# Kernel optimization log

Measured on AMD Instinct MI355X. Metric: run time of the kernel, lower is better.

The kernel has to match this reference:

```python
import jax, jax.numpy as jnp
import numpy as np

WINDOW_SIZE = 64
SHIFT_SIZE = WINDOW_SIZE // 2  # shift_windows=True
HEAD_DIM = 64
SCALE = HEAD_DIM ** (-0.5)


def _shift_mask(W):
    # static shift-window mask, computed with numpy (all shapes static)
    img_mask = np.zeros((W,), dtype=np.float32)
    cnt = 0
    for s in (slice(0, -WINDOW_SIZE), slice(-WINDOW_SIZE, -SHIFT_SIZE), slice(-SHIFT_SIZE, None)):
        img_mask[s] = cnt
        cnt += 1
    mw = img_mask.reshape(W // WINDOW_SIZE, WINDOW_SIZE)  # (num_win, ws)
    mask = mw[:, None, :] - mw[:, :, None]                # (num_win, ws, ws)
    mask = np.where(mask != 0.0, -100.0, 0.0).astype(np.float32)
    return jnp.asarray(mask)


def setup_inputs() -> dict:
    key = jax.random.key(0)
    k1, k2, k3, k4 = jax.random.split(key, 4)
    B, W, C = 32, 8192, HEAD_DIM
    return {
        "q": jax.random.normal(k1, (B, W, C), dtype=jnp.float32),
        "k": jax.random.normal(k2, (B, W, C), dtype=jnp.float32),
        "v": jax.random.normal(k3, (B, W, C), dtype=jnp.float32),
        "rel_pos_table": jax.random.normal(k4, (2 * WINDOW_SIZE - 1, 1), dtype=jnp.float32) * 0.02,
    }


def reference(q, k, v, rel_pos_table):
    B, W, C = q.shape
    ws = WINDOW_SIZE
    # relative position bias gather: (1, ws, ws)
    coords = jnp.arange(ws)
    rel_idx = coords[None, :] * 0 + (coords[:, None] - coords[None, :]) + (ws - 1)  # (ws, ws)
    bias = rel_pos_table[rel_idx.reshape(-1)].reshape(ws, ws, -1)
    bias = jnp.transpose(bias, (2, 0, 1))  # (1, ws, ws)

    mask = _shift_mask(W)  # (num_win, ws, ws)

    # cyclic shift
    q = jnp.roll(q, shift=-SHIFT_SIZE, axis=1)
    k = jnp.roll(k, shift=-SHIFT_SIZE, axis=1)
    v = jnp.roll(v, shift=-SHIFT_SIZE, axis=1)

    # window partition -> (B * num_win, ws, C)
    num_win = W // ws
    qw = q.reshape(B * num_win, ws, C)
    kw = k.reshape(B * num_win, ws, C)
    vw = v.reshape(B * num_win, ws, C)

    attn = jnp.einsum('bnc,bmc->bnm', qw, kw) * SCALE + bias  # (B*nw, ws, ws)
    attn = attn.reshape(B, num_win, ws, ws) + mask[None]
    attn = attn.reshape(-1, ws, ws)
    attn = jax.nn.softmax(attn, axis=-1)

    xw = jnp.einsum('bnm,bmc->bnc', attn, vw)  # (B*nw, ws, C)
    x = xw.reshape(B, W, C)
    x = jnp.roll(x, shift=SHIFT_SIZE, axis=1)
    return (x, attn)
```

## Files before the change

kernel.cpp:

```cpp
#include <hip/hip_runtime.h>
#include <cstdint>
#include <cstddef>

#define WS 64
#define SHIFT 32
#define WTOT 8192
#define NWIN 128
#define SCALE_F 0.125f

typedef __bf16 bf16x8 __attribute__((ext_vector_type(8)));
typedef float f32x4 __attribute__((ext_vector_type(4)));

__device__ __forceinline__ unsigned short f2bf(float f) {
  unsigned int u = __builtin_bit_cast(unsigned int, f);
  u += 0x7FFFu + ((u >> 16) & 1u);
  return (unsigned short)(u >> 16);
}
__device__ __forceinline__ float bf2f(unsigned short h) {
  unsigned int u = ((unsigned int)h) << 16;
  return __builtin_bit_cast(float, u);
}

__global__ __launch_bounds__(256, 3) void win_attn(
    const float* __restrict__ q, const float* __restrict__ k,
    const float* __restrict__ v, const float* __restrict__ table,
    float* __restrict__ xout, float* __restrict__ attn_out) {
  __shared__ __align__(16) unsigned short s_qhi[WS * WS];
  __shared__ __align__(16) unsigned short s_qlo[WS * WS];
  __shared__ __align__(16) unsigned short s_khi[WS * WS];
  __shared__ __align__(16) unsigned short s_klo[WS * WS];
  __shared__ __align__(16) unsigned short s_vthi[WS * WS];
  __shared__ __align__(16) unsigned short s_vtlo[WS * WS];
  __shared__ float s_bias[2 * WS - 1];

  const int t = threadIdx.x;
  const int b = blockIdx.x;
  const int batch = b >> 7;
  const int win = b & (NWIN - 1);

  if (t < 2 * WS - 1) s_bias[t] = table[t];

  {
    const int lr = t >> 2;
    const int lc = (t & 3) << 4;
    const int grow = (win * WS + lr + SHIFT) & (WTOT - 1);
    const size_t gbase = ((size_t)batch * WTOT + grow) * WS + lc;
#pragma unroll
    for (int i = 0; i < 16; i += 4) {
      const float4 qv = *(const float4*)(q + gbase + i);
      const float4 kv = *(const float4*)(k + gbase + i);
      const float4 vv = *(const float4*)(v + gbase + i);
      const float qa[4] = {qv.x, qv.y, qv.z, qv.w};
      const float ka[4] = {kv.x, kv.y, kv.z, kv.w};
      const float va[4] = {vv.x, vv.y, vv.z, vv.w};
#pragma unroll
      for (int e = 0; e < 4; ++e) {
        const int cc = lc + i + e;
        unsigned short h;
        h = f2bf(qa[e]);
        s_qhi[lr * WS + cc] = h;
        s_qlo[lr * WS + cc] = f2bf(qa[e] - bf2f(h));
        h = f2bf(ka[e]);
        s_khi[lr * WS + cc] = h;
        s_klo[lr * WS + cc] = f2bf(ka[e] - bf2f(h));
        h = f2bf(va[e]);
        s_vthi[cc * WS + lr] = h;
        s_vtlo[cc * WS + lr] = f2bf(va[e] - bf2f(h));
      }
    }
  }
  __syncthreads();

  const int lane = t & 63;
  const int wave = t >> 6;
  const int lrow = lane & 15;
  const int quad = lane >> 4;

  const f32x4 z4 = {0.f, 0.f, 0.f, 0.f};
  f32x4 acc[4] = {z4, z4, z4, z4};
#pragma unroll
  for (int kh = 0; kh < 2; ++kh) {
    const int k0 = kh * 32 + quad * 8;
    const bf16x8 ahi = *(const bf16x8*)(s_qhi + (wave * 16 + lrow) * WS + k0);
    const bf16x8 alo = *(const bf16x8*)(s_qlo + (wave * 16 + lrow) * WS + k0);
#pragma unroll
    for (int j = 0; j < 4; ++j) {
      const bf16x8 bhi = *(const bf16x8*)(s_khi + (j * 16 + lrow) * WS + k0);
      const bf16x8 blo = *(const bf16x8*)(s_klo + (j * 16 + lrow) * WS + k0);
      acc[j] = __builtin_amdgcn_mfma_f32_16x16x32_bf16(ahi, bhi, acc[j], 0, 0, 0);
      acc[j] = __builtin_amdgcn_mfma_f32_16x16x32_bf16(alo, bhi, acc[j], 0, 0, 0);
      acc[j] = __builtin_amdgcn_mfma_f32_16x16x32_bf16(ahi, blo, acc[j], 0, 0, 0);
    }
  }

  const bool masked = (win == NWIN - 1);
  float p[4][4];
#pragma unroll
  for (int reg = 0; reg < 4; ++reg) {
    const int r = wave * 16 + quad * 4 + reg;
    float val[4];
    float vmax = -1e30f;
#pragma unroll
    for (int j = 0; j < 4; ++j) {
      const int m = j * 16 + lrow;
      float s = acc[j][reg] * SCALE_F + s_bias[r - m + (WS - 1)];
      if (masked && (((r ^ m) & 32) != 0)) s -= 100.0f;
      val[j] = s;
      vmax = fmaxf(vmax, s);
    }
#pragma unroll
    for (int off = 1; off < 16; off <<= 1)
      vmax = fmaxf(vmax, __shfl_xor(vmax, off, 64));
    float sum = 0.f;
#pragma unroll
    for (int j = 0; j < 4; ++j) {
      val[j] = __expf(val[j] - vmax);
      sum += val[j];
    }
#pragma unroll
    for (int off = 1; off < 16; off <<= 1)
      sum += __shfl_xor(sum, off, 64);
    const float inv = 1.0f / sum;
#pragma unroll
    for (int j = 0; j < 4; ++j) p[reg][j] = val[j] * inv;
  }

  {
    float* arow = attn_out + (size_t)b * (WS * WS);
#pragma unroll
    for (int reg = 0; reg < 4; ++reg) {
      const int r = wave * 16 + quad * 4 + reg;
#pragma unroll
      for (int j = 0; j < 4; ++j) {
        const int m = j * 16 + lrow;
        const float pv = p[reg][j];
        arow[r * WS + m] = pv;
        const unsigned short h = f2bf(pv);
        s_qhi[r * WS + m] = h;
        s_qlo[r * WS + m] = f2bf(pv - bf2f(h));
      }
    }
  }
  __syncthreads();

  f32x4 xacc[4] = {z4, z4, z4, z4};
#pragma unroll
  for (int kh = 0; kh < 2; ++kh) {
    const int k0 = kh * 32 + quad * 8;
    const bf16x8 phi = *(const bf16x8*)(s_qhi + (wave * 16 + lrow) * WS + k0);
    const bf16x8 plo = *(const bf16x8*)(s_qlo + (wave * 16 + lrow) * WS + k0);
#pragma unroll
    for (int j = 0; j < 4; ++j) {
      const bf16x8 vhi = *(const bf16x8*)(s_vthi + (j * 16 + lrow) * WS + k0);
      const bf16x8 vlo = *(const bf16x8*)(s_vtlo + (j * 16 + lrow) * WS + k0);
      xacc[j] = __builtin_amdgcn_mfma_f32_16x16x32_bf16(phi, vhi, xacc[j], 0, 0, 0);
      xacc[j] = __builtin_amdgcn_mfma_f32_16x16x32_bf16(plo, vhi, xacc[j], 0, 0, 0);
      xacc[j] = __builtin_amdgcn_mfma_f32_16x16x32_bf16(phi, vlo, xacc[j], 0, 0, 0);
    }
  }

#pragma unroll
  for (int reg = 0; reg < 4; ++reg) {
    const int r = wave * 16 + quad * 4 + reg;
    const int gr = (win * WS + r + SHIFT) & (WTOT - 1);
    float* xrow = xout + ((size_t)batch * WTOT + gr) * WS;
#pragma unroll
    for (int j = 0; j < 4; ++j) {
      xrow[j * 16 + lrow] = xacc[j][reg];
    }
  }
}

extern "C" void kernel_launch(void* const* d_in, const int* in_sizes, int n_in,
                              void* d_out, int out_size, void* d_ws, size_t ws_size,
                              hipStream_t stream) {
  (void)in_sizes; (void)n_in; (void)out_size; (void)d_ws; (void)ws_size;
  const float* q = (const float*)d_in[0];
  const float* k = (const float*)d_in[1];
  const float* v = (const float*)d_in[2];
  const float* table = (const float*)d_in[3];
  float* xout = (float*)d_out;
  float* attn = (float*)d_out + (size_t)32 * WTOT * WS;
  win_attn<<<dim3(4096), dim3(256), 0, stream>>>(q, k, v, table, xout, attn);
}
```

Baseline: 284.0 us.

## Load Q directly into registers, pad LDS rows, truncate bf16 split, nontemporal stores

Q fragments are loaded from global memory straight into MFMA operand registers, so Q no longer goes through shared memory and the LDS footprint shrinks. K and V^T hi/lo tiles use a padded row stride to reduce bank conflicts, and K is written with vectorized 16-byte stores. The bf16 hi/lo split now truncates instead of rounding, which cuts conversion ALU work. The P matrix reuses the K buffer after a barrier, the target occupancy is raised to 4 blocks per CU, and output and attention stores are nontemporal. Truncation slightly changes the split-precision error, and global Q loads become per-lane 32-byte strided reads.

```diff
diff --git a/kernel.cpp b/kernel.cpp
--- a/kernel.cpp
+++ b/kernel.cpp
@@ -7,30 +7,38 @@
 #define WTOT 8192
 #define NWIN 128
 #define SCALE_F 0.125f
+#define LDS_STRIDE 72
 
 typedef __bf16 bf16x8 __attribute__((ext_vector_type(8)));
+typedef unsigned short u16x8 __attribute__((ext_vector_type(8)));
 typedef float f32x4 __attribute__((ext_vector_type(4)));
 
-__device__ __forceinline__ unsigned short f2bf(float f) {
-  unsigned int u = __builtin_bit_cast(unsigned int, f);
-  u += 0x7FFFu + ((u >> 16) & 1u);
-  return (unsigned short)(u >> 16);
-}
-__device__ __forceinline__ float bf2f(unsigned short h) {
-  unsigned int u = ((unsigned int)h) << 16;
-  return __builtin_bit_cast(float, u);
-}
-
-__global__ __launch_bounds__(256, 3) void win_attn(
+__device__ __forceinline__ void split1(float f, unsigned short& h, unsigned short& l) {
+  const unsigned u = __builtin_bit_cast(unsigned, f);
+  h = (unsigned short)(u >> 16);
+  const float hf = __builtin_bit_cast(float, u & 0xFFFF0000u);
+  const float r = f - hf;
+  l = (unsigned short)(__builtin_bit_cast(unsigned, r) >> 16);
+}
+
+__device__ __forceinline__ void split8(const float* f, bf16x8& hi, bf16x8& lo) {
+  u16x8 hv, lv;
+#pragma unroll
+  for (int e = 0; e < 8; ++e) {
+    unsigned short hh, ll;
+    split1(f[e], hh, ll);
+    hv[e] = hh; lv[e] = ll;
+  }
+  hi = __builtin_bit_cast(bf16x8, hv);
+  lo = __builtin_bit_cast(bf16x8, lv);
+}
+
+__global__ __launch_bounds__(256, 4) void win_attn(
     const float* __restrict__ q, const float* __restrict__ k,
     const float* __restrict__ v, const float* __restrict__ table,
     float* __restrict__ xout, float* __restrict__ attn_out) {
-  __shared__ __align__(16) unsigned short s_qhi[WS * WS];
-  __shared__ __align__(16) unsigned short s_qlo[WS * WS];
-  __shared__ __align__(16) unsigned short s_khi[WS * WS];
-  __shared__ __align__(16) unsigned short s_klo[WS * WS];
-  __shared__ __align__(16) unsigned short s_vthi[WS * WS];
-  __shared__ __align__(16) unsigned short s_vtlo[WS * WS];
+  __shared__ __align__(16) unsigned short s_k[2][WS * LDS_STRIDE];
+  __shared__ __align__(16) unsigned short s_vt[2][WS * LDS_STRIDE];
   __shared__ float s_bias[2 * WS - 1];
 
   const int t = threadIdx.x;
@@ -38,55 +46,73 @@
   const int batch = b >> 7;
   const int win = b & (NWIN - 1);
 
-  if (t < 2 * WS - 1) s_bias[t] = table[t];
-
-  {
-    const int lr = t >> 2;
-    const int lc = (t & 3) << 4;
-    const int grow = (win * WS + lr + SHIFT) & (WTOT - 1);
-    const size_t gbase = ((size_t)batch * WTOT + grow) * WS + lc;
-#pragma unroll
-    for (int i = 0; i < 16; i += 4) {
-      const float4 qv = *(const float4*)(q + gbase + i);
-      const float4 kv = *(const float4*)(k + gbase + i);
-      const float4 vv = *(const float4*)(v + gbase + i);
-      const float qa[4] = {qv.x, qv.y, qv.z, qv.w};
-      const float ka[4] = {kv.x, kv.y, kv.z, kv.w};
-      const float va[4] = {vv.x, vv.y, vv.z, vv.w};
-#pragma unroll
-      for (int e = 0; e < 4; ++e) {
-        const int cc = lc + i + e;
-        unsigned short h;
-        h = f2bf(qa[e]);
-        s_qhi[lr * WS + cc] = h;
-        s_qlo[lr * WS + cc] = f2bf(qa[e] - bf2f(h));
-        h = f2bf(ka[e]);
-        s_khi[lr * WS + cc] = h;
-        s_klo[lr * WS + cc] = f2bf(ka[e] - bf2f(h));
-        h = f2bf(va[e]);
-        s_vthi[cc * WS + lr] = h;
-        s_vtlo[cc * WS + lr] = f2bf(va[e] - bf2f(h));
-      }
-    }
-  }
-  __syncthreads();
-
   const int lane = t & 63;
   const int wave = t >> 6;
   const int lrow = lane & 15;
   const int quad = lane >> 4;
 
+  if (t < 2 * WS - 1) s_bias[t] = table[t];
+
+  bf16x8 aq_hi[2], aq_lo[2];
+  {
+    const int qrow = wave * 16 + lrow;
+    const int gq = (win * WS + qrow + SHIFT) & (WTOT - 1);
+    const float* qp = q + ((size_t)batch * WTOT + gq) * WS;
+#pragma unroll
+    for (int kh = 0; kh < 2; ++kh) {
+      const float4 f0 = *(const float4*)(qp + kh * 32 + quad * 8);
+      const float4 f1 = *(const float4*)(qp + kh * 32 + quad * 8 + 4);
+      const float fa[8] = {f0.x, f0.y, f0.z, f0.w, f1.x, f1.y, f1.z, f1.w};
+      split8(fa, aq_hi[kh], aq_lo[kh]);
+    }
+  }
+
+  {
+    const int lr = t >> 2;
+    const int gk = (win * WS + lr + SHIFT) & (WTOT - 1);
+    const size_t gbase = ((size_t)batch * WTOT + gk) * WS;
+
+    const int lck = (t & 3) << 4;
+    const float* kp = k + gbase + lck;
+#pragma unroll
+    for (int g = 0; g < 2; ++g) {
+      const float4 f0 = *(const float4*)(kp + g * 8);
+      const float4 f1 = *(const float4*)(kp + g * 8 + 4);
+      const float fa[8] = {f0.x, f0.y, f0.z, f0.w, f1.x, f1.y, f1.z, f1.w};
+      bf16x8 hi, lo;
+      split8(fa, hi, lo);
+      *(bf16x8*)(&s_k[0][lr * LDS_STRIDE + lck + g * 8]) = hi;
+      *(bf16x8*)(&s_k[1][lr * LDS_STRIDE + lck + g * 8]) = lo;
+    }
+
+    const int cv = (t & 3) << 2;
+#pragma unroll
+    for (int blk = 0; blk < 4; ++blk) {
+      const float4 vv = *(const float4*)(v + gbase + cv + blk * 16);
+      const float va[4] = {vv.x, vv.y, vv.z, vv.w};
+#pragma unroll
+      for (int e = 0; e < 4; ++e) {
+        const int cc = cv + blk * 16 + e;
+        unsigned short h, l;
+        split1(va[e], h, l);
+        s_vt[0][cc * LDS_STRIDE + lr] = h;
+        s_vt[1][cc * LDS_STRIDE + lr] = l;
+      }
+    }
+  }
+  __syncthreads();
+
   const f32x4 z4 = {0.f, 0.f, 0.f, 0.f};
   f32x4 acc[4] = {z4, z4, z4, z4};
 #pragma unroll
   for (int kh = 0; kh < 2; ++kh) {
+    const bf16x8 ahi = aq_hi[kh];
+    const bf16x8 alo = aq_lo[kh];
     const int k0 = kh * 32 + quad * 8;
-    const bf16x8 ahi = *(const bf16x8*)(s_qhi + (wave * 16 + lrow) * WS + k0);
-    const bf16x8 alo = *(const bf16x8*)(s_qlo + (wave * 16 + lrow) * WS + k0);
-#pragma unroll
-    for (int j = 0; j < 4; ++j) {
-      const bf16x8 bhi = *(const bf16x8*)(s_khi + (j * 16 + lrow) * WS + k0);
-      const bf16x8 blo = *(const bf16x8*)(s_klo + (j * 16 + lrow) * WS + k0);
+#pragma unroll
+    for (int j = 0; j < 4; ++j) {
+      const bf16x8 bhi = *(const bf16x8*)(&s_k[0][(j * 16 + lrow) * LDS_STRIDE + k0]);
+      const bf16x8 blo = *(const bf16x8*)(&s_k[1][(j * 16 + lrow) * LDS_STRIDE + k0]);
       acc[j] = __builtin_amdgcn_mfma_f32_16x16x32_bf16(ahi, bhi, acc[j], 0, 0, 0);
       acc[j] = __builtin_amdgcn_mfma_f32_16x16x32_bf16(alo, bhi, acc[j], 0, 0, 0);
       acc[j] = __builtin_amdgcn_mfma_f32_16x16x32_bf16(ahi, blo, acc[j], 0, 0, 0);
@@ -133,26 +159,36 @@
 #pragma unroll
       for (int j = 0; j < 4; ++j) {
         const int m = j * 16 + lrow;
-        const float pv = p[reg][j];
-        arow[r * WS + m] = pv;
-        const unsigned short h = f2bf(pv);
-        s_qhi[r * WS + m] = h;
-        s_qlo[r * WS + m] = f2bf(pv - bf2f(h));
+        __builtin_nontemporal_store(p[reg][j], arow + r * WS + m);
       }
     }
   }
+
   __syncthreads();
+
+#pragma unroll
+  for (int reg = 0; reg < 4; ++reg) {
+    const int r = wave * 16 + quad * 4 + reg;
+#pragma unroll
+    for (int j = 0; j < 4; ++j) {
+      const int m = j * 16 + lrow;
+      unsigned short h, l;
+      split1(p[reg][j], h, l);
+      s_k[0][r * LDS_STRIDE + m] = h;
+      s_k[1][r * LDS_STRIDE + m] = l;
+    }
+  }
 
   f32x4 xacc[4] = {z4, z4, z4, z4};
 #pragma unroll
   for (int kh = 0; kh < 2; ++kh) {
     const int k0 = kh * 32 + quad * 8;
-    const bf16x8 phi = *(const bf16x8*)(s_qhi + (wave * 16 + lrow) * WS + k0);
-    const bf16x8 plo = *(const bf16x8*)(s_qlo + (wave * 16 + lrow) * WS + k0);
-#pragma unroll
-    for (int j = 0; j < 4; ++j) {
-      const bf16x8 vhi = *(const bf16x8*)(s_vthi + (j * 16 + lrow) * WS + k0);
-      const bf16x8 vlo = *(const bf16x8*)(s_vtlo + (j * 16 + lrow) * WS + k0);
+    const bf16x8 phi = *(const bf16x8*)(&s_k[0][(wave * 16 + lrow) * LDS_STRIDE + k0]);
+    const bf16x8 plo = *(const bf16x8*)(&s_k[1][(wave * 16 + lrow) * LDS_STRIDE + k0]);
+#pragma unroll
+    for (int j = 0; j < 4; ++j) {
+      const bf16x8 vhi = *(const bf16x8*)(&s_vt[0][(j * 16 + lrow) * LDS_STRIDE + k0]);
+      const bf16x8 vlo = *(const bf16x8*)(&s_vt[1][(j * 16 + lrow) * LDS_STRIDE + k0]);
       xacc[j] = __builtin_amdgcn_mfma_f32_16x16x32_bf16(phi, vhi, xacc[j], 0, 0, 0);
       xacc[j] = __builtin_amdgcn_mfma_f32_16x16x32_bf16(plo, vhi, xacc[j], 0, 0, 0);
       xacc[j] = __builtin_amdgcn_mfma_f32_16x16x32_bf16(phi, vlo, xacc[j], 0, 0, 0);
@@ -166,7 +202,7 @@
     float* xrow = xout + ((size_t)batch * WTOT + gr) * WS;
 #pragma unroll
     for (int j = 0; j < 4; ++j) {
-      xrow[j * 16 + lrow] = xacc[j][reg];
+      __builtin_nontemporal_store(xacc[j][reg], xrow + j * 16 + lrow);
     }
   }
 }
```

After: 286.8 us. Within noise of the previous version (+1.0%).
